# Performance work log

Hardware: AMD Instinct MI355X
Metric: run time of the kernel (lower is better)

The kernel has to match this reference:

```python
import jax, jax.numpy as jnp
import numpy as np

B, S, D, F, E, K = 2, 2048, 1024, 4096, 8, 2


def setup_inputs() -> dict:
    key = jax.random.key(0)
    ks = jax.random.split(key, 6)
    s = 0.02  # init scale
    return {
        "x": jax.random.normal(ks[0], (B, S, D), dtype=jnp.float32),
        "Wr": jax.random.normal(ks[1], (D, E), dtype=jnp.float32) * s,
        "br": jnp.zeros((E,), dtype=jnp.float32),
        "W1": jax.random.normal(ks[2], (E, D, F), dtype=jnp.float32) * s,
        "b1": jnp.zeros((E, F), dtype=jnp.float32),
        "W2": jax.random.normal(ks[3], (E, F, D), dtype=jnp.float32) * s,
        "b2": jnp.zeros((E, D), dtype=jnp.float32),
        "top_k": K,
    }


def reference(x, Wr, br, W1, b1, W2, b2, top_k):
    b, s, d = x.shape
    e = Wr.shape[1]
    xt = x.reshape(-1, d)                              # [T, D], T = b*s
    logits = xt @ Wr + br                              # [T, E]
    probs = jax.nn.softmax(logits, axis=-1)            # [T, E] router probabilities
    topw, topi = jax.lax.top_k(probs, top_k)           # [T, K] each
    # combine weight per (token, expert): weight if expert in token's top-k else 0
    cw = jnp.sum(jax.nn.one_hot(topi, e, dtype=x.dtype) * topw[..., None], axis=1)  # [T, E]
    # dense grouped FFN: every expert over every token, then weighted combine
    h = jax.nn.relu(jnp.einsum('td,edf->tef', xt, W1) + b1)   # [T, E, F]
    y = jnp.einsum('tef,efd->ted', h, W2) + b2                # [T, E, D]
    out = jnp.einsum('te,ted->td', cw, y).reshape(b, s, d)    # [B, S, D]
    return out, probs.reshape(b, s, e)
```

## Files before the change

kernel.cpp:

```cpp
#include <hip/hip_runtime.h>
#include <hip/hip_bf16.h>


#define T_TOK 4096
#define D_DIM 1024
#define F_DIM 4096
#define E_NUM 8
#define CAP_ROWS 9216
#define N_TILES (CAP_ROWS/128)

typedef __attribute__((ext_vector_type(8))) short short8v;
typedef __attribute__((ext_vector_type(8))) unsigned short ushort8v;
typedef __attribute__((ext_vector_type(4))) float f32x4;

static __device__ __forceinline__ unsigned short f2bf(float f){
  union { float f; unsigned u; } v; v.f = f;
  unsigned r = (v.u + 0x7fffu + ((v.u >> 16) & 1u)) >> 16;
  return (unsigned short)r;
}
static __device__ __forceinline__ float bf2f(unsigned short s){
  union { unsigned u; float f; } v; v.u = ((unsigned)s) << 16;
  return v.f;
}

static __device__ __forceinline__ void gload16(const void* g, void* l) {
  __builtin_amdgcn_global_load_lds(
      (const __attribute__((address_space(1))) unsigned int*)g,
      (__attribute__((address_space(3))) unsigned int*)l, 16, 0, 0);
}

__global__ __launch_bounds__(256) void k_init(int* counts, int* cursor,
                                              int* rows_token, float* rows_w){
  const int gid = blockIdx.x * 256 + threadIdx.x;
  if (gid < E_NUM) counts[gid] = 0;
  else if (gid < 2*E_NUM) cursor[gid - E_NUM] = 0;
  if (gid < CAP_ROWS) { rows_token[gid] = 0; rows_w[gid] = 0.f; }
}

__global__ __launch_bounds__(256) void k_router(
    const float* __restrict__ x, const float* __restrict__ Wr,
    const float* __restrict__ br, float* __restrict__ probs_out,
    int* __restrict__ topi, float* __restrict__ topw, int* __restrict__ counts)
{
  const int lane = threadIdx.x & 63;
  const int t = blockIdx.x * 4 + (threadIdx.x >> 6);
  float xv[16];
  #pragma unroll
  for (int i = 0; i < 16; ++i) xv[i] = x[(size_t)t*D_DIM + i*64 + lane];
  float pe[E_NUM];
  #pragma unroll
  for (int e = 0; e < E_NUM; ++e) {
    float p = 0.f;
    #pragma unroll
    for (int i = 0; i < 16; ++i) p += xv[i] * Wr[(i*64 + lane)*E_NUM + e];
    #pragma unroll
    for (int off = 32; off >= 1; off >>= 1) p += __shfl_xor(p, off);
    pe[e] = p + br[e];
  }
  float m = pe[0];
  #pragma unroll
  for (int e = 1; e < E_NUM; ++e) m = fmaxf(m, pe[e]);
  float s = 0.f;
  #pragma unroll
  for (int e = 0; e < E_NUM; ++e) { pe[e] = expf(pe[e] - m); s += pe[e]; }
  const float inv = 1.f / s;
  int e1 = 0; float v1 = pe[0];
  #pragma unroll
  for (int e = 1; e < E_NUM; ++e) if (pe[e] > v1) { v1 = pe[e]; e1 = e; }
  int e2 = (e1 == 0) ? 1 : 0; float v2 = pe[e2];
  #pragma unroll
  for (int e = 0; e < E_NUM; ++e) if (e != e1 && pe[e] > v2) { v2 = pe[e]; e2 = e; }
  if (lane == 0) {
    #pragma unroll
    for (int e = 0; e < E_NUM; ++e) probs_out[(size_t)t*E_NUM + e] = pe[e] * inv;
    topi[t*2+0] = e1; topw[t*2+0] = v1 * inv;
    topi[t*2+1] = e2; topw[t*2+1] = v2 * inv;
    atomicAdd(&counts[e1], 1);
    atomicAdd(&counts[e2], 1);
  }
}

__global__ void k_scan(const int* __restrict__ counts, int* __restrict__ pbase,
                       int* __restrict__ tile_e)
{
  if (threadIdx.x == 0 && blockIdx.x == 0) {
    int base = 0;
    for (int e = 0; e < E_NUM; ++e) {
      pbase[e] = base;
      const int nt = (counts[e] + 127) >> 7;
      for (int i = 0; i < nt; ++i) tile_e[(base >> 7) + i] = e;
      base += nt << 7;
    }
    pbase[E_NUM] = base;
    for (int tt = base >> 7; tt < N_TILES; ++tt) tile_e[tt] = -1;
  }
}

__global__ __launch_bounds__(256) void k_assign(
    const int* __restrict__ topi, const float* __restrict__ topw,
    const int* __restrict__ pbase, int* __restrict__ cursor,
    int* __restrict__ rows_token, float* __restrict__ rows_w,
    int* __restrict__ pair_of)
{
  const int t = blockIdx.x * 256 + threadIdx.x;
  if (t < T_TOK) {
    #pragma unroll
    for (int k = 0; k < 2; ++k) {
      const int e = topi[t*2+k];
      const int slot = atomicAdd(&cursor[e], 1);
      const int pid = pbase[e] + slot;
      rows_token[pid] = t;
      rows_w[pid] = topw[t*2+k];
      pair_of[t*2+k] = pid;
    }
  }
}

__global__ __launch_bounds__(256) void k_cvt_x(const float* __restrict__ x,
                                               unsigned short* __restrict__ xbf)
{
  const int i = (blockIdx.x * 256 + threadIdx.x) * 4;
  const float4 v = *(const float4*)&x[i];
  ushort4 o; o.x=f2bf(v.x); o.y=f2bf(v.y); o.z=f2bf(v.z); o.w=f2bf(v.w);
  *(ushort4*)&xbf[i] = o;
}

template<int R, int C>
__global__ __launch_bounds__(256) void k_tcvt(const float* __restrict__ in,
                                              unsigned short* __restrict__ out)
{
  const size_t eo = (size_t)blockIdx.z * R * C;
  const int r0 = blockIdx.y * 64, c0 = blockIdx.x * 64;
  __shared__ unsigned short ls[64][66];
  const int t = threadIdx.x;
  const int rr = t >> 4, cc = (t & 15) * 4;
  #pragma unroll
  for (int p = 0; p < 4; ++p) {
    const float4 v = *(const float4*)&in[eo + (size_t)(r0 + p*16 + rr)*C + c0 + cc];
    ls[p*16+rr][cc+0]=f2bf(v.x); ls[p*16+rr][cc+1]=f2bf(v.y);
    ls[p*16+rr][cc+2]=f2bf(v.z); ls[p*16+rr][cc+3]=f2bf(v.w);
  }
  __syncthreads();
  const int kc = (t & 7) * 8, nn0 = t >> 3;
  #pragma unroll
  for (int p = 0; p < 2; ++p) {
    const int nn = nn0 + p*32;
    ushort8v o;
    #pragma unroll
    for (int j = 0; j < 8; ++j) o[j] = ls[kc + j][nn];
    *(ushort8v*)&out[eo + (size_t)(c0 + nn)*R + r0 + kc] = o;
  }
}

template<bool GATHER, int NDIM, int KDIM, bool EPI1>
__global__ __launch_bounds__(256, 2) void k_gemm(
    const unsigned short* __restrict__ A,
    const unsigned short* __restrict__ Bt,
    const float* __restrict__ bias,
    const int* __restrict__ tile_e,
    const int* __restrict__ rows_token,
    const float* __restrict__ rows_w,
    unsigned short* __restrict__ outp)
{
  const int e = tile_e[blockIdx.y];
  if (e < 0) return;
  const int rt = blockIdx.y * 128;
  const int ntc = blockIdx.x * 128;
  __shared__ __align__(16) unsigned short LB[3][2][128*32];
  const int tid = threadIdx.x;
  const int lane = tid & 63;
  const int w = tid >> 6;
  const int seg = w & 1;
  const int isB = (w >= 2) ? 1 : 0;
  const int lrow = lane >> 2, lchunk = lane & 3;
  const unsigned short* gsrc[4];
  unsigned lds_off[4];
  if (w < 2) {
    #pragma unroll
    for (int i = 0; i < 4; ++i) {
      const int rl = seg*64 + i*16 + lrow;
      const int rowidx = GATHER ? rows_token[rt + rl] : (rt + rl);
      gsrc[i] = A + (size_t)rowidx * KDIM + lchunk*8;
      lds_off[i] = (unsigned)((seg*64 + i*16)*32);
    }
  } else {
    const unsigned short* Be = Bt + (size_t)e * NDIM * KDIM;
    #pragma unroll
    for (int i = 0; i < 4; ++i) {
      const int rl = seg*64 + i*16 + lrow;
      gsrc[i] = Be + (size_t)(ntc + rl) * KDIM + lchunk*8;
      lds_off[i] = (unsigned)((seg*64 + i*16)*32);
    }
  }
  const int wr = w >> 1, wc = w & 1;
  const int cl = lane & 15, rgb = lane >> 4;
  f32x4 acc[4][4] = {};

  constexpr int NT = KDIM / 32;
  #pragma unroll
  for (int i = 0; i < 4; ++i) gload16(gsrc[i] + 0,  &LB[0][isB][lds_off[i]]);
  #pragma unroll
  for (int i = 0; i < 4; ++i) gload16(gsrc[i] + 32, &LB[1][isB][lds_off[i]]);
  asm volatile("s_waitcnt vmcnt(4)" ::: "memory");
  __builtin_amdgcn_s_barrier();

  int buf = 0;
  for (int t = 0; t < NT; ++t) {
    const int pb = (buf == 0) ? 2 : (buf - 1);
    if (t + 2 < NT) {
      const int kof = (t + 2) * 32;
      #pragma unroll
      for (int i = 0; i < 4; ++i) gload16(gsrc[i] + kof, &LB[pb][isB][lds_off[i]]);
    }
    short8v a[4], b[4];
    #pragma unroll
    for (int m = 0; m < 4; ++m)
      a[m] = *(const short8v*)&LB[buf][0][(wr*64 + m*16 + cl)*32 + rgb*8];
    #pragma unroll
    for (int n = 0; n < 4; ++n)
      b[n] = *(const short8v*)&LB[buf][1][(wc*64 + n*16 + cl)*32 + rgb*8];
    #pragma unroll
    for (int m = 0; m < 4; ++m)
      #pragma unroll
      for (int n = 0; n < 4; ++n)
        acc[m][n] = __builtin_amdgcn_mfma_f32_16x16x32_bf16(a[m], b[n], acc[m][n], 0, 0, 0);
    if (t + 2 < NT) {
      asm volatile("s_waitcnt vmcnt(4)" ::: "memory");
    } else {
      asm volatile("s_waitcnt vmcnt(0)" ::: "memory");
    }
    __builtin_amdgcn_s_barrier();
    buf = (buf == 2) ? 0 : (buf + 1);
  }

  const size_t ebias = (size_t)e * NDIM;
  #pragma unroll
  for (int n = 0; n < 4; ++n) {
    const int col = ntc + wc*64 + n*16 + cl;
    const float bv = bias[ebias + col];
    #pragma unroll
    for (int m = 0; m < 4; ++m) {
      const int row = rt + wr*64 + m*16 + rgb*4;
      #pragma unroll
      for (int r = 0; r < 4; ++r) {
        float v = acc[m][n][r] + bv;
        if (EPI1) v = fmaxf(v, 0.f);
        else      v *= rows_w[row + r];
        const unsigned short hb = f2bf(v);
        const unsigned short ob = (unsigned short)__shfl_xor((int)(unsigned)hb, 1);
        if ((lane & 1) == 0) {
          const unsigned pk = (unsigned)hb | ((unsigned)ob << 16);
          *(unsigned*)&outp[(size_t)(row + r)*NDIM + col] = pk;
        }
      }
    }
  }
}

__global__ __launch_bounds__(256) void k_combine(
    const unsigned short* __restrict__ y, const int* __restrict__ pair_of,
    float* __restrict__ out)
{
  const int gid = blockIdx.x * 256 + threadIdx.x;
  const int t = gid >> 7;
  const int c = (gid & 127) * 8;
  const int p0 = pair_of[t*2+0];
  const int p1 = pair_of[t*2+1];
  const ushort8v a = *(const ushort8v*)&y[(size_t)p0*D_DIM + c];
  const ushort8v b = *(const ushort8v*)&y[(size_t)p1*D_DIM + c];
  float o[8];
  #pragma unroll
  for (int j = 0; j < 8; ++j) o[j] = bf2f(a[j]) + bf2f(b[j]);
  float4 o0; o0.x=o[0]; o0.y=o[1]; o0.z=o[2]; o0.w=o[3];
  float4 o1; o1.x=o[4]; o1.y=o[5]; o1.z=o[6]; o1.w=o[7];
  *(float4*)&out[(size_t)t*D_DIM + c]     = o0;
  *(float4*)&out[(size_t)t*D_DIM + c + 4] = o1;
}

extern "C" void kernel_launch(void* const* d_in, const int* in_sizes, int n_in,
                              void* d_out, int out_size, void* d_ws, size_t ws_size,
                              hipStream_t stream)
{
  const float* x  = (const float*)d_in[0];
  const float* Wr = (const float*)d_in[1];
  const float* br = (const float*)d_in[2];
  const float* W1 = (const float*)d_in[3];
  const float* b1 = (const float*)d_in[4];
  const float* W2 = (const float*)d_in[5];
  const float* b2 = (const float*)d_in[6];
  (void)in_sizes; (void)n_in; (void)out_size; (void)ws_size;

  float* out   = (float*)d_out;
  float* probs = out + (size_t)T_TOK * D_DIM;

  char* w = (char*)d_ws;
  size_t off = 0;
  int*   counts     = (int*)(w + off); off += 256;
  int*   cursor     = (int*)(w + off); off += 256;
  int*   pbase      = (int*)(w + off); off += 512;
  int*   tile_e     = (int*)(w + off); off += 3072;
  int*   topi       = (int*)(w + off); off += (size_t)T_TOK*2*4;
  float* topw       = (float*)(w + off); off += (size_t)T_TOK*2*4;
  int*   pair_of    = (int*)(w + off); off += (size_t)T_TOK*2*4;
  int*   rows_token = (int*)(w + off); off += (size_t)CAP_ROWS*4;
  float* rows_w     = (float*)(w + off); off += (size_t)CAP_ROWS*4;
  off = (off + 255) & ~(size_t)255;
  unsigned short* xbf = (unsigned short*)(w + off); off += (size_t)T_TOK*D_DIM*2;
  unsigned short* Wt  = (unsigned short*)(w + off); off += (size_t)E_NUM*D_DIM*F_DIM*2;
  unsigned short* h   = (unsigned short*)(w + off); off += (size_t)CAP_ROWS*F_DIM*2;
  unsigned short* y   = (unsigned short*)(w + off); off += (size_t)CAP_ROWS*D_DIM*2;

  k_init<<<(CAP_ROWS + 255) / 256, 256, 0, stream>>>(counts, cursor, rows_token, rows_w);
  k_router<<<T_TOK / 4, 256, 0, stream>>>(x, Wr, br, probs, topi, topw, counts);
  k_scan<<<1, 64, 0, stream>>>(counts, pbase, tile_e);
  k_assign<<<T_TOK / 256, 256, 0, stream>>>(topi, topw, pbase, cursor,
                                            rows_token, rows_w, pair_of);
  k_cvt_x<<<T_TOK * D_DIM / 4 / 256, 256, 0, stream>>>(x, xbf);
  k_tcvt<D_DIM, F_DIM><<<dim3(F_DIM/64, D_DIM/64, E_NUM), 256, 0, stream>>>(W1, Wt);
  k_gemm<true, F_DIM, D_DIM, true><<<dim3(F_DIM/128, N_TILES), 256, 0, stream>>>(
      xbf, Wt, b1, tile_e, rows_token, rows_w, h);
  k_tcvt<F_DIM, D_DIM><<<dim3(D_DIM/64, F_DIM/64, E_NUM), 256, 0, stream>>>(W2, Wt);
  k_gemm<false, D_DIM, F_DIM, false><<<dim3(D_DIM/128, N_TILES), 256, 0, stream>>>(
      h, Wt, b2, tile_e, rows_token, rows_w, y);
  k_combine<<<T_TOK * D_DIM / 8 / 256, 256, 0, stream>>>(y, pair_of, out);
}
```

Before: 466.5 us.

## Enlarge grouped GEMM tiles to 256 rows with swizzled LDS and 512 threads

```diff
diff --git a/kernel.cpp b/kernel.cpp
--- a/kernel.cpp
+++ b/kernel.cpp
@@ -6,8 +6,8 @@
 #define D_DIM 1024
 #define F_DIM 4096
 #define E_NUM 8
-#define CAP_ROWS 9216
-#define N_TILES (CAP_ROWS/128)
+#define CAP_ROWS 10240
+#define N_TILES (CAP_ROWS/256)
 
 typedef __attribute__((ext_vector_type(8))) short short8v;
 typedef __attribute__((ext_vector_type(8))) unsigned short ushort8v;
@@ -40,13 +40,16 @@
 __global__ __launch_bounds__(256) void k_router(
     const float* __restrict__ x, const float* __restrict__ Wr,
     const float* __restrict__ br, float* __restrict__ probs_out,
-    int* __restrict__ topi, float* __restrict__ topw, int* __restrict__ counts)
+    int* __restrict__ topi, float* __restrict__ topw, int* __restrict__ counts,
+    unsigned short* __restrict__ xbf)
 {
   const int lane = threadIdx.x & 63;
   const int t = blockIdx.x * 4 + (threadIdx.x >> 6);
   float xv[16];
   #pragma unroll
   for (int i = 0; i < 16; ++i) xv[i] = x[(size_t)t*D_DIM + i*64 + lane];
+  #pragma unroll
+  for (int i = 0; i < 16; ++i) xbf[(size_t)t*D_DIM + i*64 + lane] = f2bf(xv[i]);
   float pe[E_NUM];
   #pragma unroll
   for (int e = 0; e < E_NUM; ++e) {
@@ -87,12 +90,12 @@
     int base = 0;
     for (int e = 0; e < E_NUM; ++e) {
       pbase[e] = base;
-      const int nt = (counts[e] + 127) >> 7;
-      for (int i = 0; i < nt; ++i) tile_e[(base >> 7) + i] = e;
-      base += nt << 7;
+      const int nt = (counts[e] + 255) >> 8;
+      for (int i = 0; i < nt; ++i) tile_e[(base >> 8) + i] = e;
+      base += nt << 8;
     }
     pbase[E_NUM] = base;
-    for (int tt = base >> 7; tt < N_TILES; ++tt) tile_e[tt] = -1;
+    for (int tt = base >> 8; tt < N_TILES; ++tt) tile_e[tt] = -1;
   }
 }
 
@@ -116,15 +119,6 @@
   }
 }
 
-__global__ __launch_bounds__(256) void k_cvt_x(const float* __restrict__ x,
-                                               unsigned short* __restrict__ xbf)
-{
-  const int i = (blockIdx.x * 256 + threadIdx.x) * 4;
-  const float4 v = *(const float4*)&x[i];
-  ushort4 o; o.x=f2bf(v.x); o.y=f2bf(v.y); o.z=f2bf(v.z); o.w=f2bf(v.w);
-  *(ushort4*)&xbf[i] = o;
-}
-
 template<int R, int C>
 __global__ __launch_bounds__(256) void k_tcvt(const float* __restrict__ in,
                                               unsigned short* __restrict__ out)
@@ -152,8 +146,8 @@
   }
 }
 
-template<bool GATHER, int NDIM, int KDIM, bool EPI1>
-__global__ __launch_bounds__(256, 2) void k_gemm(
+template<int BN, bool GATHER, int NDIM, int KT, int EPI>
+__global__ __launch_bounds__(512, 2) void k_gemm(
     const unsigned short* __restrict__ A,
     const unsigned short* __restrict__ Bt,
     const float* __restrict__ bias,
@@ -162,95 +156,130 @@
     const float* __restrict__ rows_w,
     unsigned short* __restrict__ outp)
 {
-  const int e = tile_e[blockIdx.y];
+  constexpr int KDIM = KT * 64;
+  constexpr int NB = BN / 64;
+  constexpr int NCB = BN / 32;
+  const int tot = gridDim.x * gridDim.y;
+  int flat = blockIdx.x * gridDim.y + blockIdx.y;
+  flat = (flat & 7) * (tot >> 3) + (flat >> 3);
+  const int bx = flat / gridDim.y;
+  const int by = flat % gridDim.y;
+  const int e = tile_e[by];
   if (e < 0) return;
-  const int rt = blockIdx.y * 128;
-  const int ntc = blockIdx.x * 128;
-  __shared__ __align__(16) unsigned short LB[3][2][128*32];
+  const int rt = by * 256;
+  const int ntc = bx * BN;
+  __shared__ __align__(16) unsigned short As[2 * 256 * 64];
+  __shared__ __align__(16) unsigned short Bs[2 * BN * 64];
   const int tid = threadIdx.x;
   const int lane = tid & 63;
   const int w = tid >> 6;
-  const int seg = w & 1;
-  const int isB = (w >= 2) ? 1 : 0;
-  const int lrow = lane >> 2, lchunk = lane & 3;
-  const unsigned short* gsrc[4];
-  unsigned lds_off[4];
-  if (w < 2) {
-    #pragma unroll
-    for (int i = 0; i < 4; ++i) {
-      const int rl = seg*64 + i*16 + lrow;
+  const int lr = lane >> 3;
+  const int g  = (lane & 7) ^ lr;
+  const unsigned short* gsrc[8];
+  unsigned soff[8];
+  if (w < 4) {
+    #pragma unroll
+    for (int i = 0; i < 8; ++i) {
+      const int rl = i*32 + w*8 + lr;
       const int rowidx = GATHER ? rows_token[rt + rl] : (rt + rl);
-      gsrc[i] = A + (size_t)rowidx * KDIM + lchunk*8;
-      lds_off[i] = (unsigned)((seg*64 + i*16)*32);
+      gsrc[i] = A + (size_t)rowidx * KDIM + g*8;
+      soff[i] = (unsigned)((i*32 + w*8) * 64);
     }
   } else {
     const unsigned short* Be = Bt + (size_t)e * NDIM * KDIM;
     #pragma unroll
-    for (int i = 0; i < 4; ++i) {
-      const int rl = seg*64 + i*16 + lrow;
-      gsrc[i] = Be + (size_t)(ntc + rl) * KDIM + lchunk*8;
-      lds_off[i] = (unsigned)((seg*64 + i*16)*32);
-    }
-  }
-  const int wr = w >> 1, wc = w & 1;
+    for (int i = 0; i < NCB; ++i) {
+      const int rl = i*32 + (w-4)*8 + lr;
+      gsrc[i] = Be + (size_t)(ntc + rl) * KDIM + g*8;
+      soff[i] = (unsigned)((i*32 + (w-4)*8) * 64);
+    }
+  }
+  const int wr = w >> 2, wc = w & 3;
   const int cl = lane & 15, rgb = lane >> 4;
-  f32x4 acc[4][4] = {};
-
-  constexpr int NT = KDIM / 32;
-  #pragma unroll
-  for (int i = 0; i < 4; ++i) gload16(gsrc[i] + 0,  &LB[0][isB][lds_off[i]]);
-  #pragma unroll
-  for (int i = 0; i < 4; ++i) gload16(gsrc[i] + 32, &LB[1][isB][lds_off[i]]);
-  asm volatile("s_waitcnt vmcnt(4)" ::: "memory");
+  const int swz = cl & 7;
+  f32x4 acc[8][NB] = {};
+
+  if (w < 4) {
+    #pragma unroll
+    for (int i = 0; i < 8; ++i) gload16(gsrc[i], As + soff[i]);
+    #pragma unroll
+    for (int i = 0; i < 8; ++i) gload16(gsrc[i] + 64, As + 256*64 + soff[i]);
+    asm volatile("s_waitcnt vmcnt(8)" ::: "memory");
+  } else {
+    #pragma unroll
+    for (int i = 0; i < NCB; ++i) gload16(gsrc[i], Bs + soff[i]);
+    #pragma unroll
+    for (int i = 0; i < NCB; ++i) gload16(gsrc[i] + 64, Bs + BN*64 + soff[i]);
+    if constexpr (BN == 256) { asm volatile("s_waitcnt vmcnt(8)" ::: "memory"); }
+    else                     { asm volatile("s_waitcnt vmcnt(4)" ::: "memory"); }
+  }
   __builtin_amdgcn_s_barrier();
-
-  int buf = 0;
-  for (int t = 0; t < NT; ++t) {
-    const int pb = (buf == 0) ? 2 : (buf - 1);
-    if (t + 2 < NT) {
-      const int kof = (t + 2) * 32;
+  __builtin_amdgcn_sched_barrier(0);
+
+  for (int t = 0; t < KT; ++t) {
+    const unsigned short* Ab = As + (t & 1) * (256*64);
+    const unsigned short* Bb = Bs + (t & 1) * (BN*64);
+    #pragma unroll
+    for (int ks = 0; ks < 2; ++ks) {
+      short8v a[8], b[NB];
+      const int ch = ((ks*4 + rgb) ^ swz) * 8;
       #pragma unroll
-      for (int i = 0; i < 4; ++i) gload16(gsrc[i] + kof, &LB[pb][isB][lds_off[i]]);
-    }
-    short8v a[4], b[4];
-    #pragma unroll
-    for (int m = 0; m < 4; ++m)
-      a[m] = *(const short8v*)&LB[buf][0][(wr*64 + m*16 + cl)*32 + rgb*8];
-    #pragma unroll
-    for (int n = 0; n < 4; ++n)
-      b[n] = *(const short8v*)&LB[buf][1][(wc*64 + n*16 + cl)*32 + rgb*8];
-    #pragma unroll
-    for (int m = 0; m < 4; ++m)
+      for (int m = 0; m < 8; ++m)
+        a[m] = *(const short8v*)&Ab[(wr*128 + m*16 + cl) * 64 + ch];
       #pragma unroll
-      for (int n = 0; n < 4; ++n)
-        acc[m][n] = __builtin_amdgcn_mfma_f32_16x16x32_bf16(a[m], b[n], acc[m][n], 0, 0, 0);
-    if (t + 2 < NT) {
-      asm volatile("s_waitcnt vmcnt(4)" ::: "memory");
+      for (int n = 0; n < NB; ++n)
+        b[n] = *(const short8v*)&Bb[(wc*(BN/4) + n*16 + cl) * 64 + ch];
+      __builtin_amdgcn_s_setprio(1);
+      #pragma unroll
+      for (int m = 0; m < 8; ++m)
+        #pragma unroll
+        for (int n = 0; n < NB; ++n)
+          acc[m][n] = __builtin_amdgcn_mfma_f32_16x16x32_bf16(a[m], b[n], acc[m][n], 0, 0, 0);
+      __builtin_amdgcn_s_setprio(0);
+    }
+    asm volatile("s_waitcnt lgkmcnt(0)" ::: "memory");
+    __builtin_amdgcn_sched_barrier(0);
+    __builtin_amdgcn_s_barrier();
+    __builtin_amdgcn_sched_barrier(0);
+    if (t + 2 < KT) {
+      const int ko = (t + 2) * 64;
+      if (w < 4) {
+        #pragma unroll
+        for (int i = 0; i < 8; ++i) gload16(gsrc[i] + ko, As + (t&1)*(256*64) + soff[i]);
+        asm volatile("s_waitcnt vmcnt(8)" ::: "memory");
+      } else {
+        #pragma unroll
+        for (int i = 0; i < NCB; ++i) gload16(gsrc[i] + ko, Bs + (t&1)*(BN*64) + soff[i]);
+        if constexpr (BN == 256) { asm volatile("s_waitcnt vmcnt(8)" ::: "memory"); }
+        else                     { asm volatile("s_waitcnt vmcnt(4)" ::: "memory"); }
+      }
     } else {
       asm volatile("s_waitcnt vmcnt(0)" ::: "memory");
     }
     __builtin_amdgcn_s_barrier();
-    buf = (buf == 2) ? 0 : (buf + 1);
+    __builtin_amdgcn_sched_barrier(0);
   }
 
   const size_t ebias = (size_t)e * NDIM;
   #pragma unroll
-  for (int n = 0; n < 4; ++n) {
-    const int col = ntc + wc*64 + n*16 + cl;
-    const float bv = bias[ebias + col];
-    #pragma unroll
-    for (int m = 0; m < 4; ++m) {
-      const int row = rt + wr*64 + m*16 + rgb*4;
+  for (int m = 0; m < 8; ++m) {
+    const int row = rt + wr*128 + m*16 + rgb*4;
+    float4 rw4 = make_float4(0,0,0,0);
+    if (EPI == 2) rw4 = *(const float4*)&rows_w[row];
+    #pragma unroll
+    for (int n = 0; n < NB; ++n) {
+      const int col = ntc + wc*(BN/4) + n*16 + cl;
+      const float bv = bias[ebias + col];
       #pragma unroll
       for (int r = 0; r < 4; ++r) {
         float v = acc[m][n][r] + bv;
-        if (EPI1) v = fmaxf(v, 0.f);
-        else      v *= rows_w[row + r];
+        if (EPI == 1) v = fmaxf(v, 0.f);
+        else          v *= ((const float*)&rw4)[r];
         const unsigned short hb = f2bf(v);
         const unsigned short ob = (unsigned short)__shfl_xor((int)(unsigned)hb, 1);
         if ((lane & 1) == 0) {
-          const unsigned pk = (unsigned)hb | ((unsigned)ob << 16);
-          *(unsigned*)&outp[(size_t)(row + r)*NDIM + col] = pk;
+          *(unsigned*)&outp[(size_t)(row + r) * NDIM + col] =
+              (unsigned)hb | ((unsigned)ob << 16);
         }
       }
     }
@@ -311,16 +340,15 @@
   unsigned short* y   = (unsigned short*)(w + off); off += (size_t)CAP_ROWS*D_DIM*2;
 
   k_init<<<(CAP_ROWS + 255) / 256, 256, 0, stream>>>(counts, cursor, rows_token, rows_w);
-  k_router<<<T_TOK / 4, 256, 0, stream>>>(x, Wr, br, probs, topi, topw, counts);
+  k_router<<<T_TOK / 4, 256, 0, stream>>>(x, Wr, br, probs, topi, topw, counts, xbf);
   k_scan<<<1, 64, 0, stream>>>(counts, pbase, tile_e);
   k_assign<<<T_TOK / 256, 256, 0, stream>>>(topi, topw, pbase, cursor,
                                             rows_token, rows_w, pair_of);
-  k_cvt_x<<<T_TOK * D_DIM / 4 / 256, 256, 0, stream>>>(x, xbf);
   k_tcvt<D_DIM, F_DIM><<<dim3(F_DIM/64, D_DIM/64, E_NUM), 256, 0, stream>>>(W1, Wt);
-  k_gemm<true, F_DIM, D_DIM, true><<<dim3(F_DIM/128, N_TILES), 256, 0, stream>>>(
+  k_gemm<256, true, F_DIM, 16, 1><<<dim3(F_DIM/256, N_TILES), 512, 0, stream>>>(
       xbf, Wt, b1, tile_e, rows_token, rows_w, h);
   k_tcvt<F_DIM, D_DIM><<<dim3(D_DIM/64, F_DIM/64, E_NUM), 256, 0, stream>>>(W2, Wt);
-  k_gemm<false, D_DIM, F_DIM, false><<<dim3(D_DIM/128, N_TILES), 256, 0, stream>>>(
+  k_gemm<128, false, D_DIM, 64, 2><<<dim3(D_DIM/128, N_TILES), 512, 0, stream>>>(
       h, Wt, b2, tile_e, rows_token, rows_w, y);
   k_combine<<<T_TOK * D_DIM / 8 / 256, 256, 0, stream>>>(y, pair_of, out);
 }
```

Measured after the change: 566.1 us. 21.3% more time.
